# Kernel tuning notes

Measured on AMD Instinct MI355X. Metric: run time of the kernel, lower is better.

## Reference

```python
import jax, jax.numpy as jnp
import numpy as np

B, T, D_IN = 2, 2048, 1024
H, D_HEAD = 16, 64
D_INNER = H * D_HEAD  # 1024
D_OUT = D_HEAD        # out_proj maps d_inner -> d_out


def setup_inputs() -> dict:
    key = jax.random.key(0)
    ks = jax.random.split(key, 6)
    s_in = 1.0 / np.sqrt(D_IN)
    s_inner = 1.0 / np.sqrt(D_INNER)
    return {
        "x": jax.random.normal(ks[0], (B, T, D_IN), dtype=jnp.float32),
        "Wq": jax.random.uniform(ks[1], (D_IN, D_INNER), jnp.float32, -s_in, s_in),
        "Wk": jax.random.uniform(ks[2], (D_IN, D_INNER), jnp.float32, -s_in, s_in),
        "Wv": jax.random.uniform(ks[3], (D_IN, D_INNER), jnp.float32, -s_in, s_in),
        "Wo": jax.random.uniform(ks[4], (D_INNER, D_OUT), jnp.float32, -s_inner, s_inner),
        "bo": jax.random.uniform(ks[5], (D_OUT,), jnp.float32, -s_inner, s_inner),
    }


def reference(x, Wq, Wk, Wv, Wo, bo):
    b, t, _ = x.shape
    # projections -> [b, h, t, d]
    def split_heads(y):
        return y.reshape(b, t, H, D_HEAD).transpose(0, 2, 1, 3)
    q = split_heads(x @ Wq)
    k = split_heads(x @ Wk)
    v = split_heads(x @ Wv)
    scores = jnp.einsum("bhqd,bhkd->bhqk", q, k)
    causal = jnp.triu(jnp.ones((t, t), dtype=bool), k=1)
    scores = jnp.where(causal, -jnp.inf, scores)
    # NOTE: original scales by sqrt(d_out*num_heads), not sqrt(head_dim)
    attn = jax.nn.softmax(scores / np.sqrt(D_INNER), axis=-1)
    y = jnp.einsum("bhqk,bhkd->bhqd", attn, v)
    y = y.transpose(0, 2, 1, 3).reshape(b, t, D_INNER)
    return y @ Wo + bo
```

## Files before the change

kernel.cpp:

```cpp
#include <hip/hip_runtime.h>

typedef __attribute__((ext_vector_type(8))) short short8;
typedef __attribute__((ext_vector_type(4))) float f32x4;
typedef __attribute__((ext_vector_type(8))) unsigned short ushort8v;


__device__ __forceinline__ unsigned short f2bf(float f) {
  union { float f; unsigned int u; } x; x.f = f;
  unsigned int r = x.u + 0x7FFFu + ((x.u >> 16) & 1u);
  return (unsigned short)(r >> 16);
}

__device__ __forceinline__ void gload_lds16(const void* g, void* l) {
  __builtin_amdgcn_global_load_lds(
      (const __attribute__((address_space(1))) void*)g,
      (__attribute__((address_space(3))) void*)l, 16, 0, 0);
}


__global__ __launch_bounds__(256) void prep(
    const float* __restrict__ x,
    const float* __restrict__ Wq, const float* __restrict__ Wk, const float* __restrict__ Wv,
    const float* __restrict__ Wo, const float* __restrict__ bo,
    unsigned short* __restrict__ xb,
    unsigned short* __restrict__ wqt, unsigned short* __restrict__ wkt,
    unsigned short* __restrict__ wvt, unsigned short* __restrict__ wot,
    float* __restrict__ out) {
  __shared__ float tile[32][33];
  int b = blockIdx.x;
  if (b < 4096) {
    int i = (b * 256 + threadIdx.x) * 4;
    float4 f = *(const float4*)(x + i);
    ushort4 o;
    o.x = f2bf(f.x); o.y = f2bf(f.y); o.z = f2bf(f.z); o.w = f2bf(f.w);
    *(ushort4*)(xb + i) = o;
  } else if (b < 7168) {
    int idx = b - 4096;
    int z = idx >> 10, rem = idx & 1023;
    const float* src = (z == 0) ? Wq : (z == 1) ? Wk : Wv;
    unsigned short* dst = (z == 0) ? wqt : (z == 1) ? wkt : wvt;
    int kx = (rem & 31) * 32, ny = (rem >> 5) * 32;
    int tx = threadIdx.x & 31, ty = threadIdx.x >> 5;
    #pragma unroll
    for (int r = 0; r < 32; r += 8)
      tile[ty + r][tx] = src[(size_t)(kx + ty + r) * 1024 + ny + tx];
    __syncthreads();
    #pragma unroll
    for (int r = 0; r < 32; r += 8)
      dst[(size_t)(ny + ty + r) * 1024 + kx + tx] = f2bf(tile[tx][ty + r]);
  } else if (b < 7232) {
    int idx = b - 7168;
    int kx = (idx & 31) * 32, ny = (idx >> 5) * 32;
    int tx = threadIdx.x & 31, ty = threadIdx.x >> 5;
    #pragma unroll
    for (int r = 0; r < 32; r += 8)
      tile[ty + r][tx] = Wo[(size_t)(kx + ty + r) * 64 + ny + tx];
    __syncthreads();
    #pragma unroll
    for (int r = 0; r < 32; r += 8)
      wot[(size_t)(ny + ty + r) * 1024 + kx + tx] = f2bf(tile[tx][ty + r]);
  } else {
    int t = (b - 7232) * 256 + threadIdx.x;
    float4 bi = *(const float4*)(bo + (t & 15) * 4);
    *(float4*)(out + (size_t)t * 4) = bi;
  }
}


__global__ __launch_bounds__(256) void qkv_gemm(
    const unsigned short* __restrict__ Xb,
    const unsigned short* __restrict__ Wqt, const unsigned short* __restrict__ Wkt,
    const unsigned short* __restrict__ Wvt,
    unsigned short* __restrict__ Oq, unsigned short* __restrict__ Ok,
    unsigned short* __restrict__ Ovt) {
  constexpr int Kd = 1024;
  __shared__ __align__(16) unsigned short As[128 * 64];
  __shared__ __align__(16) unsigned short Bs[128 * 64];
  int z = blockIdx.z;
  int m0, n0;
  const unsigned short *Arow, *Brow;
  if (z == 2) {
    m0 = blockIdx.y * 128; n0 = blockIdx.x * 128;
    Arow = Wvt; Brow = Xb;
  } else {
    m0 = blockIdx.x * 128; n0 = blockIdx.y * 128;
    Arow = Xb; Brow = (z == 0) ? Wqt : Wkt;
  }
  int tid = threadIdx.x, lane = tid & 63, wave = tid >> 6;
  int wm = wave >> 1, wn = wave & 1;
  int l15 = lane & 15, quad = lane >> 4;
  int swz = l15 & 7;

  f32x4 acc[4][4] = {};

  for (int k0 = 0; k0 < Kd; k0 += 64) {
    __syncthreads();
    #pragma unroll
    for (int r = 0; r < 4; ++r) {
      int i = tid + 256 * r;
      int row = i >> 3, c8 = i & 7;
      int gc8 = c8 ^ (row & 7);
      gload_lds16(Arow + (size_t)(m0 + row) * Kd + k0 + gc8 * 8, &As[i * 8]);
    }
    #pragma unroll
    for (int r = 0; r < 4; ++r) {
      int i = tid + 256 * r;
      int row = i >> 3, c8 = i & 7;
      int gc8 = c8 ^ (row & 7);
      gload_lds16(Brow + (size_t)(n0 + row) * Kd + k0 + gc8 * 8, &Bs[i * 8]);
    }
    __syncthreads();
    short8 af[4][2], bf[4][2];
    #pragma unroll
    for (int s = 0; s < 2; ++s) {
      #pragma unroll
      for (int i = 0; i < 4; ++i)
        af[i][s] = *(const short8*)&As[(wm * 64 + i * 16 + l15) * 64 + (((s << 2) + quad) ^ swz) * 8];
      #pragma unroll
      for (int j = 0; j < 4; ++j)
        bf[j][s] = *(const short8*)&Bs[(wn * 64 + j * 16 + l15) * 64 + (((s << 2) + quad) ^ swz) * 8];
    }
    #pragma unroll
    for (int s = 0; s < 2; ++s)
      #pragma unroll
      for (int i = 0; i < 4; ++i)
        #pragma unroll
        for (int j = 0; j < 4; ++j)
          acc[i][j] = __builtin_amdgcn_mfma_f32_16x16x32_bf16(af[i][s], bf[j][s], acc[i][j], 0, 0, 0);
  }

  if (z == 2) {
    #pragma unroll
    for (int i = 0; i < 4; ++i) {
      int dmbase = m0 + wm * 64 + i * 16 + quad * 4;
      #pragma unroll
      for (int j = 0; j < 4; ++j) {
        int tn = n0 + wn * 64 + j * 16 + l15;
        int b = tn >> 11, t = tn & 2047;
        #pragma unroll
        for (int r = 0; r < 4; ++r) {
          int dm = dmbase + r;
          int h = dm >> 6, d = dm & 63;
          Ovt[(((size_t)(b * 16 + h) * 64 + d) << 11) + t] = f2bf(acc[i][j][r]);
        }
      }
    }
  } else {
    unsigned short* O = (z == 0) ? Oq : Ok;
    float scale = (z == 0) ? 0.03125f : 1.0f;
    #pragma unroll
    for (int i = 0; i < 4; ++i) {
      int mbase = m0 + wm * 64 + i * 16 + quad * 4;
      #pragma unroll
      for (int j = 0; j < 4; ++j) {
        int n = n0 + wn * 64 + j * 16 + l15;
        int h = n >> 6, d = n & 63;
        #pragma unroll
        for (int r = 0; r < 4; ++r) {
          int mm = mbase + r;
          int b = mm >> 11, t = mm & 2047;
          size_t off = (((size_t)(b * 16 + h) * 2048 + t) << 6) + d;
          O[off] = f2bf(acc[i][j][r] * scale);
        }
      }
    }
  }
}


__global__ __launch_bounds__(256, 2) void attn8(
    const unsigned short* __restrict__ Qg, const unsigned short* __restrict__ Kg,
    const unsigned short* __restrict__ Vtg, unsigned short* __restrict__ Yg) {
  constexpr int T = 2048;
  __shared__ __align__(16) unsigned short Ks[64 * 72];
  __shared__ __align__(16) unsigned short Vs[64 * 72];
  __shared__ __align__(16) unsigned short Ps[4][32 * 72];
  int bi = blockIdx.x;
  int half = bi >> 8, idx = bi & 255;
  int bh = idx & 31;
  int t8 = idx >> 5;
  int qt = half ? (7 - t8) : (8 + t8);
  int tid = threadIdx.x, lane = tid & 63, wave = tid >> 6;
  int l15 = lane & 15, quad = lane >> 4;
  const unsigned short* Qb = Qg + (size_t)bh * T * 64;
  const unsigned short* Kb = Kg + (size_t)bh * T * 64;
  const unsigned short* Vb = Vtg + (size_t)bh * 64 * T;
  int h = bh & 15, b = bh >> 4;
  int qw = qt * 128 + wave * 32;

  short8 qf[2][2];
  #pragma unroll
  for (int jq = 0; jq < 2; ++jq)
    #pragma unroll
    for (int s = 0; s < 2; ++s)
      qf[jq][s] = *(const short8*)(Qb + (size_t)(qw + jq * 16 + l15) * 64 + quad * 8 + 32 * s);

  f32x4 Oacc[2][4] = {};
  float m_run[2] = {-__builtin_inff(), -__builtin_inff()};
  float l_run[2] = {0.f, 0.f};

  int ntrip = 2 * qt + 2;

  ushort8v kpre[2], vpre[2];
  #pragma unroll
  for (int r = 0; r < 2; ++r) {
    int i = tid + 256 * r;
    kpre[r] = *(const ushort8v*)(Kb + (size_t)(i >> 3) * 64 + (i & 7) * 8);
    vpre[r] = *(const ushort8v*)(Vb + (size_t)(i >> 3) * T + (i & 7) * 8);
  }

  for (int kt = 0; kt < ntrip; ++kt) {
    __syncthreads();
    #pragma unroll
    for (int r = 0; r < 2; ++r) {
      int i = tid + 256 * r;
      *(ushort8v*)&Ks[(i >> 3) * 72 + (i & 7) * 8] = kpre[r];
      *(ushort8v*)&Vs[(i >> 3) * 72 + (i & 7) * 8] = vpre[r];
    }
    __syncthreads();
    if (kt + 1 < ntrip) {
      #pragma unroll
      for (int r = 0; r < 2; ++r) {
        int i = tid + 256 * r;
        kpre[r] = *(const ushort8v*)(Kb + (size_t)((kt + 1) * 64 + (i >> 3)) * 64 + (i & 7) * 8);
        vpre[r] = *(const ushort8v*)(Vb + (size_t)(i >> 3) * T + (kt + 1) * 64 + (i & 7) * 8);
      }
    }

    if (kt * 64 > qw + 31) continue;

    f32x4 S[4][2] = {};
    #pragma unroll
    for (int s = 0; s < 2; ++s)
      #pragma unroll
      for (int mi = 0; mi < 4; ++mi) {
        short8 kf = *(const short8*)&Ks[(mi * 16 + l15) * 72 + quad * 8 + 32 * s];
        #pragma unroll
        for (int jq = 0; jq < 2; ++jq)
          S[mi][jq] = __builtin_amdgcn_mfma_f32_16x16x32_bf16(kf, qf[jq][s], S[mi][jq], 0, 0, 0);
      }

    if (kt * 64 + 63 > qw) {
      #pragma unroll
      for (int mi = 0; mi < 4; ++mi) {
        int tok = kt * 64 + mi * 16 + quad * 4;
        #pragma unroll
        for (int jq = 0; jq < 2; ++jq) {
          int q = qw + jq * 16 + l15;
          #pragma unroll
          for (int r = 0; r < 4; ++r)
            if (tok + r > q) S[mi][jq][r] = -__builtin_inff();
        }
      }
    }

    float alpha[2];
    #pragma unroll
    for (int jq = 0; jq < 2; ++jq) {
      float vmax = -__builtin_inff();
      #pragma unroll
      for (int mi = 0; mi < 4; ++mi)
        #pragma unroll
        for (int r = 0; r < 4; ++r)
          vmax = fmaxf(vmax, S[mi][jq][r]);
      vmax = fmaxf(vmax, __shfl_xor(vmax, 16));
      vmax = fmaxf(vmax, __shfl_xor(vmax, 32));
      float mnew = fmaxf(m_run[jq], vmax);
      alpha[jq] = __expf(m_run[jq] - mnew);
      m_run[jq] = mnew;
      float rs = 0.f;
      #pragma unroll
      for (int mi = 0; mi < 4; ++mi) {
        float p0 = __expf(S[mi][jq][0] - mnew);
        float p1 = __expf(S[mi][jq][1] - mnew);
        float p2 = __expf(S[mi][jq][2] - mnew);
        float p3 = __expf(S[mi][jq][3] - mnew);
        rs += (p0 + p1) + (p2 + p3);
        union { float f; unsigned int u; } a0{p0}, a1{p1}, a2{p2}, a3{p3};
        uint2 pk;
        pk.x = ((a0.u + 0x8000u) >> 16) | ((a1.u + 0x8000u) & 0xFFFF0000u);
        pk.y = ((a2.u + 0x8000u) >> 16) | ((a3.u + 0x8000u) & 0xFFFF0000u);
        *(uint2*)&Ps[wave][(jq * 16 + l15) * 72 + mi * 16 + quad * 4] = pk;
      }
      rs += __shfl_xor(rs, 16);
      rs += __shfl_xor(rs, 32);
      l_run[jq] = l_run[jq] * alpha[jq] + rs;
    }

    #pragma unroll
    for (int jq = 0; jq < 2; ++jq)
      #pragma unroll
      for (int jd = 0; jd < 4; ++jd)
        #pragma unroll
        for (int r = 0; r < 4; ++r)
          Oacc[jq][jd][r] *= alpha[jq];

    #pragma unroll
    for (int s = 0; s < 2; ++s) {
      short8 vfr[4];
      #pragma unroll
      for (int jd = 0; jd < 4; ++jd)
        vfr[jd] = *(const short8*)&Vs[(jd * 16 + l15) * 72 + s * 32 + quad * 8];
      #pragma unroll
      for (int jq = 0; jq < 2; ++jq) {
        short8 pf = *(const short8*)&Ps[wave][(jq * 16 + l15) * 72 + s * 32 + quad * 8];
        #pragma unroll
        for (int jd = 0; jd < 4; ++jd)
          Oacc[jq][jd] = __builtin_amdgcn_mfma_f32_16x16x32_bf16(vfr[jd], pf, Oacc[jq][jd], 0, 0, 0);
      }
    }
  }

  #pragma unroll
  for (int jq = 0; jq < 2; ++jq) {
    float linv = 1.f / l_run[jq];
    int q = qw + jq * 16 + l15;
    size_t row = (size_t)(b * 2048 + q) * 1024 + h * 64 + quad * 4;
    #pragma unroll
    for (int jd = 0; jd < 4; ++jd) {
      union { float f; unsigned int u; } a0{Oacc[jq][jd][0] * linv}, a1{Oacc[jq][jd][1] * linv},
                                         a2{Oacc[jq][jd][2] * linv}, a3{Oacc[jq][jd][3] * linv};
      uint2 pk;
      pk.x = ((a0.u + 0x7FFFu + ((a0.u >> 16) & 1u)) >> 16) |
             ((a1.u + 0x7FFFu + ((a1.u >> 16) & 1u)) & 0xFFFF0000u);
      pk.y = ((a2.u + 0x7FFFu + ((a2.u >> 16) & 1u)) >> 16) |
             ((a3.u + 0x7FFFu + ((a3.u >> 16) & 1u)) & 0xFFFF0000u);
      *(uint2*)(Yg + row + jd * 16) = pk;
    }
  }
}


__global__ __launch_bounds__(256) void oproj(
    const unsigned short* __restrict__ Y, const unsigned short* __restrict__ Wot,
    float* __restrict__ out) {
  __shared__ __align__(16) unsigned short As[64 * 32];
  __shared__ __align__(16) unsigned short Bs[64 * 32];
  int m0 = blockIdx.x * 64;
  int kbase = blockIdx.y * 256;
  int tid = threadIdx.x, lane = tid & 63, wave = tid >> 6;
  int l15 = lane & 15, quad = lane >> 4;
  f32x4 acc[4] = {};
  for (int k0 = kbase; k0 < kbase + 256; k0 += 32) {
    __syncthreads();
    {
      int row = tid >> 2, c8 = (tid & 3) * 8;
      gload_lds16(Y + (size_t)(m0 + row) * 1024 + k0 + c8, &As[tid * 8]);
      gload_lds16(Wot + (size_t)row * 1024 + k0 + c8, &Bs[tid * 8]);
    }
    __syncthreads();
    short8 af = *(const short8*)&As[(wave * 16 + l15) * 32 + quad * 8];
    #pragma unroll
    for (int j = 0; j < 4; ++j) {
      short8 bf = *(const short8*)&Bs[(j * 16 + l15) * 32 + quad * 8];
      acc[j] = __builtin_amdgcn_mfma_f32_16x16x32_bf16(af, bf, acc[j], 0, 0, 0);
    }
  }
  #pragma unroll
  for (int j = 0; j < 4; ++j) {
    int n = j * 16 + l15;
    #pragma unroll
    for (int r = 0; r < 4; ++r) {
      int m = m0 + wave * 16 + quad * 4 + r;
      atomicAdd(&out[(size_t)m * 64 + n], acc[j][r]);
    }
  }
}


extern "C" void kernel_launch(void* const* d_in, const int* in_sizes, int n_in,
                              void* d_out, int out_size, void* d_ws, size_t ws_size,
                              hipStream_t stream) {
  const float* x  = (const float*)d_in[0];
  const float* Wq = (const float*)d_in[1];
  const float* Wk = (const float*)d_in[2];
  const float* Wv = (const float*)d_in[3];
  const float* Wo = (const float*)d_in[4];
  const float* bo = (const float*)d_in[5];
  float* out = (float*)d_out;
  char* ws = (char*)d_ws;

  unsigned short* xb  = (unsigned short*)(ws);
  unsigned short* wqt = (unsigned short*)(ws + (8ull << 20));
  unsigned short* wkt = (unsigned short*)(ws + (10ull << 20));
  unsigned short* wvt = (unsigned short*)(ws + (12ull << 20));
  unsigned short* wot = (unsigned short*)(ws + (14ull << 20));
  unsigned short* q   = (unsigned short*)(ws + (15ull << 20));
  unsigned short* k   = (unsigned short*)(ws + (23ull << 20));
  unsigned short* vt  = (unsigned short*)(ws + (31ull << 20));
  unsigned short* y   = (unsigned short*)(ws + (39ull << 20));

  prep<<<7488, 256, 0, stream>>>(x, Wq, Wk, Wv, Wo, bo, xb, wqt, wkt, wvt, wot, out);
  qkv_gemm<<<dim3(32, 8, 3), 256, 0, stream>>>(xb, wqt, wkt, wvt, q, k, vt);
  attn8<<<512, 256, 0, stream>>>(q, k, vt, y);
  oproj<<<dim3(64, 4), 256, 0, stream>>>(y, wot, out);
}
```

Baseline: 177.6 us.

## Pair complementary 64-row query tiles per block and vectorize QKV epilogue stores

```diff
diff --git a/kernel.cpp b/kernel.cpp
--- a/kernel.cpp
+++ b/kernel.cpp
@@ -80,11 +80,11 @@
   int m0, n0;
   const unsigned short *Arow, *Brow;
   if (z == 2) {
+    m0 = blockIdx.x * 128; n0 = blockIdx.y * 128;
+    Arow = Xb; Brow = Wvt;
+  } else {
     m0 = blockIdx.y * 128; n0 = blockIdx.x * 128;
-    Arow = Wvt; Brow = Xb;
-  } else {
-    m0 = blockIdx.x * 128; n0 = blockIdx.y * 128;
-    Arow = Xb; Brow = (z == 0) ? Wqt : Wkt;
+    Arow = (z == 0) ? Wqt : Wkt; Brow = Xb;
   }
   int tid = threadIdx.x, lane = tid & 63, wave = tid >> 6;
   int wm = wave >> 1, wn = wave & 1;
@@ -132,17 +132,16 @@
   if (z == 2) {
     #pragma unroll
     for (int i = 0; i < 4; ++i) {
-      int dmbase = m0 + wm * 64 + i * 16 + quad * 4;
+      int tbase = m0 + wm * 64 + i * 16 + quad * 4;
+      int b = tbase >> 11, tt = tbase & 2047;
       #pragma unroll
       for (int j = 0; j < 4; ++j) {
-        int tn = n0 + wn * 64 + j * 16 + l15;
-        int b = tn >> 11, t = tn & 2047;
-        #pragma unroll
-        for (int r = 0; r < 4; ++r) {
-          int dm = dmbase + r;
-          int h = dm >> 6, d = dm & 63;
-          Ovt[(((size_t)(b * 16 + h) * 64 + d) << 11) + t] = f2bf(acc[i][j][r]);
-        }
+        int dm = n0 + wn * 64 + j * 16 + l15;
+        int h = dm >> 6, d = dm & 63;
+        unsigned int u0 = f2bf(acc[i][j][0]), u1 = f2bf(acc[i][j][1]);
+        unsigned int u2 = f2bf(acc[i][j][2]), u3 = f2bf(acc[i][j][3]);
+        uint2 pk; pk.x = u0 | (u1 << 16); pk.y = u2 | (u3 << 16);
+        *(uint2*)(Ovt + (((size_t)(b * 16 + h) * 64 + d) << 11) + tt) = pk;
       }
     }
   } else {
@@ -150,56 +149,51 @@
     float scale = (z == 0) ? 0.03125f : 1.0f;
     #pragma unroll
     for (int i = 0; i < 4; ++i) {
-      int mbase = m0 + wm * 64 + i * 16 + quad * 4;
+      int dmbase = m0 + wm * 64 + i * 16 + quad * 4;
+      int h = dmbase >> 6, d0 = dmbase & 63;
       #pragma unroll
       for (int j = 0; j < 4; ++j) {
-        int n = n0 + wn * 64 + j * 16 + l15;
-        int h = n >> 6, d = n & 63;
-        #pragma unroll
-        for (int r = 0; r < 4; ++r) {
-          int mm = mbase + r;
-          int b = mm >> 11, t = mm & 2047;
-          size_t off = (((size_t)(b * 16 + h) * 2048 + t) << 6) + d;
-          O[off] = f2bf(acc[i][j][r] * scale);
-        }
-      }
-    }
-  }
-}
-
-
-__global__ __launch_bounds__(256, 2) void attn8(
+        int t = n0 + wn * 64 + j * 16 + l15;
+        int b = t >> 11, tt = t & 2047;
+        unsigned int u0 = f2bf(acc[i][j][0] * scale), u1 = f2bf(acc[i][j][1] * scale);
+        unsigned int u2 = f2bf(acc[i][j][2] * scale), u3 = f2bf(acc[i][j][3] * scale);
+        uint2 pk; pk.x = u0 | (u1 << 16); pk.y = u2 | (u3 << 16);
+        *(uint2*)(O + (((size_t)(b * 16 + h) * 2048 + tt) << 6) + d0) = pk;
+      }
+    }
+  }
+}
+
+
+__global__ __launch_bounds__(256, 2) void attn9(
     const unsigned short* __restrict__ Qg, const unsigned short* __restrict__ Kg,
     const unsigned short* __restrict__ Vtg, unsigned short* __restrict__ Yg) {
   constexpr int T = 2048;
   __shared__ __align__(16) unsigned short Ks[64 * 72];
   __shared__ __align__(16) unsigned short Vs[64 * 72];
   __shared__ __align__(16) unsigned short Ps[4][32 * 72];
-  int bi = blockIdx.x;
-  int half = bi >> 8, idx = bi & 255;
-  int bh = idx & 31;
-  int t8 = idx >> 5;
-  int qt = half ? (7 - t8) : (8 + t8);
+  int bh = blockIdx.x;
+  int by = blockIdx.y;
+  int pp = (by < 8) ? by : 23 - by;
+  int qtA = pp, qtB = 31 - pp;
   int tid = threadIdx.x, lane = tid & 63, wave = tid >> 6;
   int l15 = lane & 15, quad = lane >> 4;
   const unsigned short* Qb = Qg + (size_t)bh * T * 64;
   const unsigned short* Kb = Kg + (size_t)bh * T * 64;
   const unsigned short* Vb = Vtg + (size_t)bh * 64 * T;
   int h = bh & 15, b = bh >> 4;
-  int qw = qt * 128 + wave * 32;
+  int qw[2] = {qtA * 64 + wave * 16, qtB * 64 + wave * 16};
 
   short8 qf[2][2];
   #pragma unroll
   for (int jq = 0; jq < 2; ++jq)
     #pragma unroll
     for (int s = 0; s < 2; ++s)
-      qf[jq][s] = *(const short8*)(Qb + (size_t)(qw + jq * 16 + l15) * 64 + quad * 8 + 32 * s);
+      qf[jq][s] = *(const short8*)(Qb + (size_t)(qw[jq] + l15) * 64 + quad * 8 + 32 * s);
 
   f32x4 Oacc[2][4] = {};
   float m_run[2] = {-__builtin_inff(), -__builtin_inff()};
   float l_run[2] = {0.f, 0.f};
-
-  int ntrip = 2 * qt + 2;
 
   ushort8v kpre[2], vpre[2];
   #pragma unroll
@@ -209,7 +203,7 @@
     vpre[r] = *(const ushort8v*)(Vb + (size_t)(i >> 3) * T + (i & 7) * 8);
   }
 
-  for (int kt = 0; kt < ntrip; ++kt) {
+  for (int kt = 0; kt <= qtA; ++kt) {
     __syncthreads();
     #pragma unroll
     for (int r = 0; r < 2; ++r) {
@@ -218,7 +212,7 @@
       *(ushort8v*)&Vs[(i >> 3) * 72 + (i & 7) * 8] = vpre[r];
     }
     __syncthreads();
-    if (kt + 1 < ntrip) {
+    {
       #pragma unroll
       for (int r = 0; r < 2; ++r) {
         int i = tid + 256 * r;
@@ -227,8 +221,6 @@
       }
     }
 
-    if (kt * 64 > qw + 31) continue;
-
     f32x4 S[4][2] = {};
     #pragma unroll
     for (int s = 0; s < 2; ++s)
@@ -240,17 +232,14 @@
           S[mi][jq] = __builtin_amdgcn_mfma_f32_16x16x32_bf16(kf, qf[jq][s], S[mi][jq], 0, 0, 0);
       }
 
-    if (kt * 64 + 63 > qw) {
+    if (kt == qtA) {
+      int ql = wave * 16 + l15;
       #pragma unroll
       for (int mi = 0; mi < 4; ++mi) {
-        int tok = kt * 64 + mi * 16 + quad * 4;
-        #pragma unroll
-        for (int jq = 0; jq < 2; ++jq) {
-          int q = qw + jq * 16 + l15;
-          #pragma unroll
-          for (int r = 0; r < 4; ++r)
-            if (tok + r > q) S[mi][jq][r] = -__builtin_inff();
-        }
+        int tokl = mi * 16 + quad * 4;
+        #pragma unroll
+        for (int r = 0; r < 4; ++r)
+          if (tokl + r > ql) S[mi][0][r] = -__builtin_inff();
       }
     }
 
@@ -311,20 +300,100 @@
     }
   }
 
+  for (int kt = qtA + 1; kt <= qtB; ++kt) {
+    __syncthreads();
+    #pragma unroll
+    for (int r = 0; r < 2; ++r) {
+      int i = tid + 256 * r;
+      *(ushort8v*)&Ks[(i >> 3) * 72 + (i & 7) * 8] = kpre[r];
+      *(ushort8v*)&Vs[(i >> 3) * 72 + (i & 7) * 8] = vpre[r];
+    }
+    __syncthreads();
+    if (kt < qtB) {
+      #pragma unroll
+      for (int r = 0; r < 2; ++r) {
+        int i = tid + 256 * r;
+        kpre[r] = *(const ushort8v*)(Kb + (size_t)((kt + 1) * 64 + (i >> 3)) * 64 + (i & 7) * 8);
+        vpre[r] = *(const ushort8v*)(Vb + (size_t)(i >> 3) * T + (kt + 1) * 64 + (i & 7) * 8);
+      }
+    }
+
+    f32x4 S[4] = {};
+    #pragma unroll
+    for (int s = 0; s < 2; ++s)
+      #pragma unroll
+      for (int mi = 0; mi < 4; ++mi) {
+        short8 kf = *(const short8*)&Ks[(mi * 16 + l15) * 72 + quad * 8 + 32 * s];
+        S[mi] = __builtin_amdgcn_mfma_f32_16x16x32_bf16(kf, qf[1][s], S[mi], 0, 0, 0);
+      }
+
+    if (kt == qtB) {
+      int ql = wave * 16 + l15;
+      #pragma unroll
+      for (int mi = 0; mi < 4; ++mi) {
+        int tokl = mi * 16 + quad * 4;
+        #pragma unroll
+        for (int r = 0; r < 4; ++r)
+          if (tokl + r > ql) S[mi][r] = -__builtin_inff();
+      }
+    }
+
+    float vmax = -__builtin_inff();
+    #pragma unroll
+    for (int mi = 0; mi < 4; ++mi)
+      #pragma unroll
+      for (int r = 0; r < 4; ++r)
+        vmax = fmaxf(vmax, S[mi][r]);
+    vmax = fmaxf(vmax, __shfl_xor(vmax, 16));
+    vmax = fmaxf(vmax, __shfl_xor(vmax, 32));
+    float mnew = fmaxf(m_run[1], vmax);
+    float alpha = __expf(m_run[1] - mnew);
+    m_run[1] = mnew;
+    float rs = 0.f;
+    #pragma unroll
+    for (int mi = 0; mi < 4; ++mi) {
+      float p0 = __expf(S[mi][0] - mnew);
+      float p1 = __expf(S[mi][1] - mnew);
+      float p2 = __expf(S[mi][2] - mnew);
+      float p3 = __expf(S[mi][3] - mnew);
+      rs += (p0 + p1) + (p2 + p3);
+      union { float f; unsigned int u; } a0{p0}, a1{p1}, a2{p2}, a3{p3};
+      uint2 pk;
+      pk.x = ((a0.u + 0x8000u) >> 16) | ((a1.u + 0x8000u) & 0xFFFF0000u);
+      pk.y = ((a2.u + 0x8000u) >> 16) | ((a3.u + 0x8000u) & 0xFFFF0000u);
+      *(uint2*)&Ps[wave][(16 + l15) * 72 + mi * 16 + quad * 4] = pk;
+    }
+    rs += __shfl_xor(rs, 16);
+    rs += __shfl_xor(rs, 32);
+    l_run[1] = l_run[1] * alpha + rs;
+
+    #pragma unroll
+    for (int jd = 0; jd < 4; ++jd)
+      #pragma unroll
+      for (int r = 0; r < 4; ++r)
+        Oacc[1][jd][r] *= alpha;
+
+    #pragma unroll
+    for (int s = 0; s < 2; ++s) {
+      short8 pf = *(const short8*)&Ps[wave][(16 + l15) * 72 + s * 32 + quad * 8];
+      #pragma unroll
+      for (int jd = 0; jd < 4; ++jd) {
+        short8 vfr = *(const short8*)&Vs[(jd * 16 + l15) * 72 + s * 32 + quad * 8];
+        Oacc[1][jd] = __builtin_amdgcn_mfma_f32_16x16x32_bf16(vfr, pf, Oacc[1][jd], 0, 0, 0);
+      }
+    }
+  }
+
   #pragma unroll
   for (int jq = 0; jq < 2; ++jq) {
     float linv = 1.f / l_run[jq];
-    int q = qw + jq * 16 + l15;
+    int q = qw[jq] + l15;
     size_t row = (size_t)(b * 2048 + q) * 1024 + h * 64 + quad * 4;
     #pragma unroll
     for (int jd = 0; jd < 4; ++jd) {
-      union { float f; unsigned int u; } a0{Oacc[jq][jd][0] * linv}, a1{Oacc[jq][jd][1] * linv},
-                                         a2{Oacc[jq][jd][2] * linv}, a3{Oacc[jq][jd][3] * linv};
-      uint2 pk;
-      pk.x = ((a0.u + 0x7FFFu + ((a0.u >> 16) & 1u)) >> 16) |
-             ((a1.u + 0x7FFFu + ((a1.u >> 16) & 1u)) & 0xFFFF0000u);
-      pk.y = ((a2.u + 0x7FFFu + ((a2.u >> 16) & 1u)) >> 16) |
-             ((a3.u + 0x7FFFu + ((a3.u >> 16) & 1u)) & 0xFFFF0000u);
+      unsigned int u0 = f2bf(Oacc[jq][jd][0] * linv), u1 = f2bf(Oacc[jq][jd][1] * linv);
+      unsigned int u2 = f2bf(Oacc[jq][jd][2] * linv), u3 = f2bf(Oacc[jq][jd][3] * linv);
+      uint2 pk; pk.x = u0 | (u1 << 16); pk.y = u2 | (u3 << 16);
       *(uint2*)(Yg + row + jd * 16) = pk;
     }
   }
@@ -392,6 +461,6 @@
 
   prep<<<7488, 256, 0, stream>>>(x, Wq, Wk, Wv, Wo, bo, xb, wqt, wkt, wvt, wot, out);
   qkv_gemm<<<dim3(32, 8, 3), 256, 0, stream>>>(xb, wqt, wkt, wvt, q, k, vt);
-  attn8<<<512, 256, 0, stream>>>(q, k, vt, y);
+  attn9<<<dim3(32, 16), 256, 0, stream>>>(q, k, vt, y);
   oproj<<<dim3(64, 4), 256, 0, stream>>>(y, wot, out);
 }
```

After: 158.8 us. 1.12x faster.
